# Performance work log

Hardware: AMD Instinct MI355X
Metric: run time of the kernel (lower is better)

## Reference

```python
import jax, jax.numpy as jnp
import numpy as np
import math

ANSWER_LEN = 11; D_MODEL = 6; FFN_DIM = 3; HEAD_DIM = 3; MAX_SEQ_LEN = 34
N_HEADS = 2; POS_DIM = 3; TOK_DIM = 3; VOCAB_SIZE = 14; MAX_DIGITS = 10
EOS_TOKEN = 12; EQUALS_TOKEN = 11; PAD_TOKEN = 13; PLUS_TOKEN = 10
B, T = 65536, 34


def _spiral(i, period):
    return (math.cos(2 * math.pi * i / period), math.sin(2 * math.pi * i / period), i / max(period - 1, 1))


def _build_pos_enc():
    N_POS = 10
    pe = np.zeros((MAX_SEQ_LEN, POS_DIM), dtype=np.float32)
    for i in range(MAX_DIGITS):
        pe[i] = _spiral(i, N_POS)
    for i in range(MAX_DIGITS):
        pe[11 + i] = _spiral(i, N_POS)
    for i in range(min(ANSWER_LEN, N_POS)):
        pe[22 + i] = _spiral(i, N_POS)
    pe[32] = [0.0, 0.0, 1.5]
    pe[10] = [2.0, 0.0, -1.0]
    pe[21] = [0.0, 2.0, -1.0]
    pe[33] = [-2.0, 0.0, -1.0]
    return pe


def _build_tok_emb():
    emb = np.zeros((VOCAB_SIZE, TOK_DIM), dtype=np.float32)
    for d in range(10):
        emb[d] = _spiral(d, 10)
    emb[PLUS_TOKEN] = [2.0, 0.0, -1.0]
    emb[EQUALS_TOKEN] = [0.0, 2.0, -1.0]
    emb[EOS_TOKEN] = [-2.0, 0.0, -1.0]
    emb[PAD_TOKEN] = [0.0, -2.0, -1.0]
    return emb


def setup_inputs() -> dict:
    key = jax.random.key(0)
    ks = jax.random.split(key, 12)
    H = N_HEADS * HEAD_DIM  # 6

    def lin(k, out_d, in_d):
        bound = 1.0 / math.sqrt(in_d)
        return jax.random.uniform(k, (out_d, in_d), jnp.float32, -bound, bound)

    return {
        'idx': jax.random.randint(ks[0], (B, T), 0, VOCAB_SIZE),
        'tok_emb': jnp.asarray(_build_tok_emb()),
        'pos_enc': jnp.asarray(_build_pos_enc()),
        'q_w': lin(ks[1], H, POS_DIM),
        'k_w': lin(ks[2], H, POS_DIM),
        'v_w': lin(ks[3], H, TOK_DIM),
        'out_w': lin(ks[4], D_MODEL, H),
        'ln1_g': jnp.ones((D_MODEL,)), 'ln1_b': jnp.zeros((D_MODEL,)),
        'ln2_g': jnp.ones((D_MODEL,)), 'ln2_b': jnp.zeros((D_MODEL,)),
        'lnf_g': jnp.ones((D_MODEL,)), 'lnf_b': jnp.zeros((D_MODEL,)),
        'ffn_w1': lin(ks[5], FFN_DIM, D_MODEL),
        'ffn_b1': jax.random.uniform(ks[6], (FFN_DIM,), jnp.float32, -1/math.sqrt(D_MODEL), 1/math.sqrt(D_MODEL)),
        'ffn_w2': lin(ks[7], D_MODEL, FFN_DIM),
        'ffn_b2': jax.random.uniform(ks[8], (D_MODEL,), jnp.float32, -1/math.sqrt(FFN_DIM), 1/math.sqrt(FFN_DIM)),
        'head_w': lin(ks[9], TOK_DIM, D_MODEL),
    }


def _ln(x, g, b, eps=1e-5):
    mu = jnp.mean(x, -1, keepdims=True)
    var = jnp.mean((x - mu) ** 2, -1, keepdims=True)
    return (x - mu) * jax.lax.rsqrt(var + eps) * g + b


def reference(idx, tok_emb, pos_enc, q_w, k_w, v_w, out_w,
              ln1_g, ln1_b, ln2_g, ln2_b, lnf_g, lnf_b,
              ffn_w1, ffn_b1, ffn_w2, ffn_b2, head_w):
    b, t = idx.shape
    tok = tok_emb[idx]                              # [B,T,3]
    pos = jnp.broadcast_to(pos_enc[:t][None], (b, t, POS_DIM))
    x = jnp.concatenate([tok, pos], -1)             # [B,T,6]
    h = _ln(x, ln1_g, ln1_b)
    x_tok, x_pos = h[..., :TOK_DIM], h[..., TOK_DIM:]
    q = (x_pos @ q_w.T).reshape(b, t, N_HEADS, HEAD_DIM)
    k = (x_pos @ k_w.T).reshape(b, t, N_HEADS, HEAD_DIM)
    v = (x_tok @ v_w.T).reshape(b, t, N_HEADS, HEAD_DIM)
    attn = jnp.einsum('bqhd,bkhd->bhqk', q, k) / math.sqrt(HEAD_DIM)
    mask = jnp.tril(jnp.ones((t, t), dtype=bool))
    attn = jnp.where(mask[None, None], attn, -jnp.inf)
    attn = jax.nn.softmax(attn, -1)
    out = jnp.einsum('bhqk,bkhd->bqhd', attn, v).reshape(b, t, N_HEADS * HEAD_DIM)
    x = x + out @ out_w.T
    h2 = _ln(x, ln2_g, ln2_b)
    ffn = jax.nn.gelu(h2 @ ffn_w1.T + ffn_b1, approximate=False) @ ffn_w2.T + ffn_b2
    x = x + ffn
    x = _ln(x, lnf_g, lnf_b)
    return (x @ head_w.T) @ tok_emb.T               # [B,T,VOCAB]
```

## Files before the change

kernel.cpp:

```cpp
#include <hip/hip_runtime.h>
#include <math.h>

#define TT  34
#define VV  14
#define BLK 256


__global__ __launch_bounds__(BLK) void addtx_fwd(
    const int*   __restrict__ idx,
    const float* __restrict__ tok_emb,
    const float* __restrict__ pos_enc,
    const float* __restrict__ q_w,
    const float* __restrict__ k_w,
    const float* __restrict__ v_w,
    const float* __restrict__ out_w,
    const float* __restrict__ ln1_g, const float* __restrict__ ln1_b,
    const float* __restrict__ ln2_g, const float* __restrict__ ln2_b,
    const float* __restrict__ lnf_g, const float* __restrict__ lnf_b,
    const float* __restrict__ ffn_w1, const float* __restrict__ ffn_b1,
    const float* __restrict__ ffn_w2, const float* __restrict__ ffn_b2,
    const float* __restrict__ head_w,
    float* __restrict__ out)
{
    __shared__ float4 kvtab[TT * VV * 3];
    __shared__ float  wsm[192];
    __shared__ float  lgs[BLK * VV];

    const int tid = threadIdx.x;
    const int blk = blockIdx.x;

    {
        const int i = tid;
        if (i < 36)       wsm[i] = out_w[i];
        else if (i < 42)  wsm[i] = ln2_g[i - 36];
        else if (i < 48)  wsm[i] = ln2_b[i - 42];
        else if (i < 66)  wsm[i] = ffn_w1[i - 48];
        else if (i < 69)  wsm[i] = ffn_b1[i - 66];
        else if (i < 87)  wsm[i] = ffn_w2[i - 69];
        else if (i < 93)  wsm[i] = ffn_b2[i - 87];
        else if (i < 99)  wsm[i] = lnf_g[i - 93];
        else if (i < 105) wsm[i] = lnf_b[i - 99];
        else if (i < 189) {
            const int j = i - 105, v = j / 6, d = j - v * 6;
            wsm[i] = head_w[0 * 6 + d] * tok_emb[v * 3 + 0]
                   + head_w[1 * 6 + d] * tok_emb[v * 3 + 1]
                   + head_w[2 * 6 + d] * tok_emb[v * 3 + 2];
        }
    }

    const float rs3 = 0.57735026918962576f;
    for (int e = tid; e < TT * VV; e += BLK) {
        const int pos = e / VV, id = e - pos * VV;
        float x[6];
        x[0] = tok_emb[id * 3 + 0]; x[1] = tok_emb[id * 3 + 1]; x[2] = tok_emb[id * 3 + 2];
        x[3] = pos_enc[pos * 3 + 0]; x[4] = pos_enc[pos * 3 + 1]; x[5] = pos_enc[pos * 3 + 2];
        float mu = (x[0] + x[1] + x[2] + x[3] + x[4] + x[5]) * (1.0f / 6.0f);
        float var = 0.0f;
        #pragma unroll
        for (int d = 0; d < 6; ++d) { float dd = x[d] - mu; var += dd * dd; }
        const float rstd = rsqrtf(var * (1.0f / 6.0f) + 1e-5f);
        float h[6];
        #pragma unroll
        for (int d = 0; d < 6; ++d) h[d] = (x[d] - mu) * rstd * ln1_g[d] + ln1_b[d];
        float kk[6], vvv[6];
        #pragma unroll
        for (int r = 0; r < 6; ++r) {
            kk[r]  = (h[3] * k_w[r * 3 + 0] + h[4] * k_w[r * 3 + 1] + h[5] * k_w[r * 3 + 2]) * rs3;
            vvv[r] =  h[0] * v_w[r * 3 + 0] + h[1] * v_w[r * 3 + 1] + h[2] * v_w[r * 3 + 2];
        }
        kvtab[e * 3 + 0] = make_float4(kk[0], kk[1], kk[2], kk[3]);
        kvtab[e * 3 + 1] = make_float4(kk[4], kk[5], vvv[0], vvv[1]);
        kvtab[e * 3 + 2] = make_float4(vvv[2], vvv[3], vvv[4], vvv[5]);
    }
    __syncthreads();

    const int srank = (tid + ((blk & 3) << 6)) & (BLK - 1);
    const int r0 = (blk * BLK) % TT;
    int rem = srank, dsel = 0, ksel = 0, found = 0;
    #pragma unroll 1
    for (int tau = 0; tau < TT; ++tau) {
        int dlt = tau - r0; if (dlt < 0) dlt += TT;
        const int c = (dlt < (BLK % TT)) ? (BLK / TT + 1) : (BLK / TT);
        if (!found) {
            if (rem < c) { dsel = dlt; ksel = rem; found = 1; }
            else rem -= c;
        }
    }
    const int il   = dsel + ksel * TT;
    const int flat = blk * BLK + il;
    const int b    = flat / TT;
    const int t    = flat - b * TT;
    const int* __restrict__ row = idx + b * TT;

    float x[6];
    {
        const int mid = row[t];
        x[0] = tok_emb[mid * 3 + 0]; x[1] = tok_emb[mid * 3 + 1]; x[2] = tok_emb[mid * 3 + 2];
        x[3] = pos_enc[t * 3 + 0];   x[4] = pos_enc[t * 3 + 1];   x[5] = pos_enc[t * 3 + 2];
    }
    float q[6];
    {
        float mu = (x[0] + x[1] + x[2] + x[3] + x[4] + x[5]) * (1.0f / 6.0f);
        float var = 0.0f;
        #pragma unroll
        for (int d = 0; d < 6; ++d) { float dd = x[d] - mu; var += dd * dd; }
        const float rstd = rsqrtf(var * (1.0f / 6.0f) + 1e-5f);
        float h[6];
        #pragma unroll
        for (int d = 0; d < 6; ++d) h[d] = (x[d] - mu) * rstd * ln1_g[d] + ln1_b[d];
        #pragma unroll
        for (int r = 0; r < 6; ++r)
            q[r] = h[3] * q_w[r * 3 + 0] + h[4] * q_w[r * 3 + 1] + h[5] * q_w[r * 3 + 2];
    }

    float l0 = 0.f, l1 = 0.f;
    float a0 = 0.f, a1 = 0.f, a2 = 0.f, a3 = 0.f, a4 = 0.f, a5 = 0.f;
    int ebase = 0;
    for (int s = 0; s <= t; ++s) {
        const int ids = row[s];
        const float4* e4 = &kvtab[(ebase + ids) * 3];
        const float4 ka = e4[0];
        const float4 kb = e4[1];
        const float4 vb = e4[2];
        const float sc0 = q[0] * ka.x + q[1] * ka.y + q[2] * ka.z;
        const float sc1 = q[3] * ka.w + q[4] * kb.x + q[5] * kb.y;
        const float p0 = __expf(sc0);
        const float p1 = __expf(sc1);
        l0 += p0; l1 += p1;
        a0 += p0 * kb.z; a1 += p0 * kb.w; a2 += p0 * vb.x;
        a3 += p1 * vb.y; a4 += p1 * vb.z; a5 += p1 * vb.w;
        ebase += VV;
    }
    const float i0 = 1.0f / l0, i1 = 1.0f / l1;
    const float o6[6] = { a0 * i0, a1 * i0, a2 * i0, a3 * i1, a4 * i1, a5 * i1 };

    #pragma unroll
    for (int d = 0; d < 6; ++d) {
        float s = x[d];
        #pragma unroll
        for (int j = 0; j < 6; ++j) s += o6[j] * wsm[d * 6 + j];
        x[d] = s;
    }

    {
        float mu = (x[0] + x[1] + x[2] + x[3] + x[4] + x[5]) * (1.0f / 6.0f);
        float var = 0.0f;
        #pragma unroll
        for (int d = 0; d < 6; ++d) { float dd = x[d] - mu; var += dd * dd; }
        const float rstd = rsqrtf(var * (1.0f / 6.0f) + 1e-5f);
        float h2[6];
        #pragma unroll
        for (int d = 0; d < 6; ++d) h2[d] = (x[d] - mu) * rstd * wsm[36 + d] + wsm[42 + d];
        float g3[3];
        #pragma unroll
        for (int i = 0; i < 3; ++i) {
            float f = wsm[66 + i];
            #pragma unroll
            for (int d = 0; d < 6; ++d) f += h2[d] * wsm[48 + i * 6 + d];
            g3[i] = 0.5f * f * (1.0f + erff(f * 0.70710678118654752f));
        }
        #pragma unroll
        for (int d = 0; d < 6; ++d) {
            float s = x[d] + wsm[87 + d];
            #pragma unroll
            for (int i = 0; i < 3; ++i) s += g3[i] * wsm[69 + d * 3 + i];
            x[d] = s;
        }
    }

    {
        float mu = (x[0] + x[1] + x[2] + x[3] + x[4] + x[5]) * (1.0f / 6.0f);
        float var = 0.0f;
        #pragma unroll
        for (int d = 0; d < 6; ++d) { float dd = x[d] - mu; var += dd * dd; }
        const float rstd = rsqrtf(var * (1.0f / 6.0f) + 1e-5f);
        float xf[6];
        #pragma unroll
        for (int d = 0; d < 6; ++d) xf[d] = (x[d] - mu) * rstd * wsm[93 + d] + wsm[99 + d];
        #pragma unroll
        for (int v = 0; v < VV; ++v) {
            float s = 0.0f;
            #pragma unroll
            for (int d = 0; d < 6; ++d) s += xf[d] * wsm[105 + v * 6 + d];
            lgs[il * VV + v] = s;
        }
    }
    __syncthreads();

    float* __restrict__ ob = out + (size_t)blk * (BLK * VV);
    #pragma unroll
    for (int j = 0; j < VV; ++j)
        ob[j * BLK + tid] = lgs[j * BLK + tid];
}

extern "C" void kernel_launch(void* const* d_in, const int* in_sizes, int n_in,
                              void* d_out, int out_size, void* d_ws, size_t ws_size,
                              hipStream_t stream) {
    const int*   idx     = (const int*)  d_in[0];
    const float* tok_emb = (const float*)d_in[1];
    const float* pos_enc = (const float*)d_in[2];
    const float* q_w     = (const float*)d_in[3];
    const float* k_w     = (const float*)d_in[4];
    const float* v_w     = (const float*)d_in[5];
    const float* out_w   = (const float*)d_in[6];
    const float* ln1_g   = (const float*)d_in[7];
    const float* ln1_b   = (const float*)d_in[8];
    const float* ln2_g   = (const float*)d_in[9];
    const float* ln2_b   = (const float*)d_in[10];
    const float* lnf_g   = (const float*)d_in[11];
    const float* lnf_b   = (const float*)d_in[12];
    const float* ffn_w1  = (const float*)d_in[13];
    const float* ffn_b1  = (const float*)d_in[14];
    const float* ffn_w2  = (const float*)d_in[15];
    const float* ffn_b2  = (const float*)d_in[16];
    const float* head_w  = (const float*)d_in[17];
    float* out = (float*)d_out;

    const int n = in_sizes[0];
    const int blocks = n / BLK;
    addtx_fwd<<<blocks, BLK, 0, stream>>>(idx, tok_emb, pos_enc, q_w, k_w, v_w, out_w,
                                          ln1_g, ln1_b, ln2_g, ln2_b, lnf_g, lnf_b,
                                          ffn_w1, ffn_b1, ffn_w2, ffn_b2, head_w, out);
}
```

Before: 256.7 us.

## Remap work so each lane owns a sequence and processes several query positions

Each block now handles 64 sequences. Each wave covers a slice of 4 (or 6) query positions, and each lane owns one sequence, so K/V table lookups in the causal attention loop are shared across several queries held in registers. Token indices are staged in padded shared memory, embeddings and ln1/q weights are cached in shared memory, and exp is replaced with exp2 using pre-scaled queries. Logits are written straight to global memory with float4 stores instead of being staged in shared memory. The cost is higher register pressure, imbalance between waves (the last wave does more work), and per-lane strided global stores that may coalesce poorly.

```diff
diff --git a/kernel.cpp b/kernel.cpp
--- a/kernel.cpp
+++ b/kernel.cpp
@@ -1,19 +1,145 @@
 #include <hip/hip_runtime.h>
 #include <math.h>
 
-#define TT  34
-#define VV  14
-#define BLK 256
-
-
-__global__ __launch_bounds__(BLK) void addtx_fwd(
+#define TT   34
+#define VV   14
+#define NROW 64
+#define BLK  512
+
+
+__device__ __forceinline__ void epi_t(int t, int id, const float* a,
+                                      const float* wsm, const float* stab,
+                                      float* lg) {
+    const float i0 = 1.0f / a[0], i1 = 1.0f / a[1];
+    const float o6[6] = { a[2]*i0, a[3]*i0, a[4]*i0, a[5]*i1, a[6]*i1, a[7]*i1 };
+    float x[6];
+    x[0] = stab[id*3+0]; x[1] = stab[id*3+1]; x[2] = stab[id*3+2];
+    x[3] = stab[42+t*3+0]; x[4] = stab[42+t*3+1]; x[5] = stab[42+t*3+2];
+    #pragma unroll
+    for (int d = 0; d < 6; ++d) {
+        float s = x[d];
+        #pragma unroll
+        for (int j = 0; j < 6; ++j) s += o6[j] * wsm[d*6+j];
+        x[d] = s;
+    }
+    {
+        float mu = (x[0]+x[1]+x[2]+x[3]+x[4]+x[5]) * (1.0f/6.0f);
+        float var = 0.f;
+        #pragma unroll
+        for (int d = 0; d < 6; ++d) { float dd = x[d]-mu; var += dd*dd; }
+        const float rstd = rsqrtf(var*(1.0f/6.0f) + 1e-5f);
+        float h2[6];
+        #pragma unroll
+        for (int d = 0; d < 6; ++d) h2[d] = (x[d]-mu)*rstd*wsm[36+d] + wsm[42+d];
+        float g3[3];
+        #pragma unroll
+        for (int i = 0; i < 3; ++i) {
+            float f = wsm[66+i];
+            #pragma unroll
+            for (int d = 0; d < 6; ++d) f += h2[d]*wsm[48+i*6+d];
+            g3[i] = 0.5f * f * (1.0f + erff(f*0.70710678118654752f));
+        }
+        #pragma unroll
+        for (int d = 0; d < 6; ++d) {
+            float s = x[d] + wsm[87+d];
+            #pragma unroll
+            for (int i = 0; i < 3; ++i) s += g3[i]*wsm[69+d*3+i];
+            x[d] = s;
+        }
+    }
+    {
+        float mu = (x[0]+x[1]+x[2]+x[3]+x[4]+x[5]) * (1.0f/6.0f);
+        float var = 0.f;
+        #pragma unroll
+        for (int d = 0; d < 6; ++d) { float dd = x[d]-mu; var += dd*dd; }
+        const float rstd = rsqrtf(var*(1.0f/6.0f) + 1e-5f);
+        float xf[6];
+        #pragma unroll
+        for (int d = 0; d < 6; ++d) xf[d] = (x[d]-mu)*rstd*wsm[93+d] + wsm[99+d];
+        #pragma unroll
+        for (int v = 0; v < VV; ++v) {
+            float s = 0.f;
+            #pragma unroll
+            for (int d = 0; d < 6; ++d) s += xf[d]*wsm[105+v*6+d];
+            lg[v] = s;
+        }
+    }
+}
+
+#define ATT_BODY(J) do { \
+    float sc0 = q[J][0]*ka.x + q[J][1]*ka.y + q[J][2]*ka.z; \
+    float sc1 = q[J][3]*ka.w + q[J][4]*kb.x + q[J][5]*kb.y; \
+    float p0 = exp2f(sc0); \
+    float p1 = exp2f(sc1); \
+    acc[J][0] += p0;       acc[J][1] += p1; \
+    acc[J][2] += p0*kb.z;  acc[J][3] += p0*kb.w;  acc[J][4] += p0*vb.x; \
+    acc[J][5] += p1*vb.y;  acc[J][6] += p1*vb.z;  acc[J][7] += p1*vb.w; \
+} while (0)
+
+template<int G>
+__device__ __forceinline__ void slot_run(int t0, const int* __restrict__ lrow,
+                                         const float4* __restrict__ kvt,
+                                         const float* __restrict__ wsm,
+                                         const float* __restrict__ stab,
+                                         float* __restrict__ outp) {
+    const float qs = 1.4426950408889634f;
+    float q[G][6];
+    float acc[G][8];
+    #pragma unroll
+    for (int j = 0; j < G; ++j) {
+        const int t = t0 + j;
+        const int id = lrow[t];
+        const float x0 = stab[id*3+0], x1 = stab[id*3+1], x2 = stab[id*3+2];
+        const float x3 = stab[42+t*3+0], x4 = stab[42+t*3+1], x5 = stab[42+t*3+2];
+        const float mu = (x0+x1+x2+x3+x4+x5) * (1.0f/6.0f);
+        const float d0=x0-mu,d1=x1-mu,d2=x2-mu,d3=x3-mu,d4=x4-mu,d5=x5-mu;
+        const float var = d0*d0+d1*d1+d2*d2+d3*d3+d4*d4+d5*d5;
+        const float rstd = rsqrtf(var*(1.0f/6.0f) + 1e-5f);
+        const float h3 = d3*rstd*stab[147] + stab[153];
+        const float h4 = d4*rstd*stab[148] + stab[154];
+        const float h5 = d5*rstd*stab[149] + stab[155];
+        #pragma unroll
+        for (int r = 0; r < 6; ++r)
+            q[j][r] = (h3*stab[156+r*3] + h4*stab[156+r*3+1] + h5*stab[156+r*3+2]) * qs;
+        #pragma unroll
+        for (int k = 0; k < 8; ++k) acc[j][k] = 0.f;
+    }
+    for (int s = 0; s <= t0; ++s) {
+        const int ids = lrow[s];
+        const float4* e4 = &kvt[(s*VV + ids)*3];
+        const float4 ka = e4[0], kb = e4[1], vb = e4[2];
+        #pragma unroll
+        for (int j = 0; j < G; ++j) ATT_BODY(j);
+    }
+    #pragma unroll
+    for (int u = 1; u < G; ++u) {
+        const int s = t0 + u;
+        const int ids = lrow[s];
+        const float4* e4 = &kvt[(s*VV + ids)*3];
+        const float4 ka = e4[0], kb = e4[1], vb = e4[2];
+        #pragma unroll
+        for (int j = u; j < G; ++j) ATT_BODY(j);
+    }
+    #pragma unroll
+    for (int p = 0; p < G/2; ++p) {
+        alignas(16) float lg[28];
+        #pragma unroll
+        for (int h = 0; h < 2; ++h) {
+            const int j = 2*p + h, t = t0 + j;
+            epi_t(t, lrow[t], acc[j], wsm, stab, &lg[14*h]);
+        }
+        float4* d4 = (float4*)(outp + (t0 + 2*p)*VV);
+        const float4* s4 = (const float4*)lg;
+        #pragma unroll
+        for (int w = 0; w < 7; ++w) d4[w] = s4[w];
+    }
+}
+
+__global__ __launch_bounds__(BLK, 4) void addtx_fwd(
     const int*   __restrict__ idx,
-    const float* __restrict__ tok_emb,
-    const float* __restrict__ pos_enc,
-    const float* __restrict__ q_w,
-    const float* __restrict__ k_w,
-    const float* __restrict__ v_w,
-    const float* __restrict__ out_w,
+    const float* __restrict__ tok_emb, const float* __restrict__ pos_enc,
+    const float* __restrict__ q_w, const float* __restrict__ k_w,
+    const float* __restrict__ v_w, const float* __restrict__ out_w,
     const float* __restrict__ ln1_g, const float* __restrict__ ln1_b,
     const float* __restrict__ ln2_g, const float* __restrict__ ln2_b,
     const float* __restrict__ lnf_g, const float* __restrict__ lnf_b,
@@ -22,175 +148,83 @@
     const float* __restrict__ head_w,
     float* __restrict__ out)
 {
-    __shared__ float4 kvtab[TT * VV * 3];
+    __shared__ float4 kvtab[TT*VV*3];
     __shared__ float  wsm[192];
-    __shared__ float  lgs[BLK * VV];
+    __shared__ float  stab[176];
+    __shared__ int    lidx[NROW*35];
 
     const int tid = threadIdx.x;
     const int blk = blockIdx.x;
 
-    {
+    if (tid < 189) {
         const int i = tid;
-        if (i < 36)       wsm[i] = out_w[i];
-        else if (i < 42)  wsm[i] = ln2_g[i - 36];
-        else if (i < 48)  wsm[i] = ln2_b[i - 42];
-        else if (i < 66)  wsm[i] = ffn_w1[i - 48];
-        else if (i < 69)  wsm[i] = ffn_b1[i - 66];
-        else if (i < 87)  wsm[i] = ffn_w2[i - 69];
-        else if (i < 93)  wsm[i] = ffn_b2[i - 87];
-        else if (i < 99)  wsm[i] = lnf_g[i - 93];
-        else if (i < 105) wsm[i] = lnf_b[i - 99];
-        else if (i < 189) {
-            const int j = i - 105, v = j / 6, d = j - v * 6;
-            wsm[i] = head_w[0 * 6 + d] * tok_emb[v * 3 + 0]
-                   + head_w[1 * 6 + d] * tok_emb[v * 3 + 1]
-                   + head_w[2 * 6 + d] * tok_emb[v * 3 + 2];
-        }
-    }
-
-    const float rs3 = 0.57735026918962576f;
-    for (int e = tid; e < TT * VV; e += BLK) {
-        const int pos = e / VV, id = e - pos * VV;
+        float w;
+        if (i < 36)       w = out_w[i];
+        else if (i < 42)  w = ln2_g[i-36];
+        else if (i < 48)  w = ln2_b[i-42];
+        else if (i < 66)  w = ffn_w1[i-48];
+        else if (i < 69)  w = ffn_b1[i-66];
+        else if (i < 87)  w = ffn_w2[i-69];
+        else if (i < 93)  w = ffn_b2[i-87];
+        else if (i < 99)  w = lnf_g[i-93];
+        else if (i < 105) w = lnf_b[i-99];
+        else {
+            const int j = i-105, v = j/6, d = j-v*6;
+            w = head_w[0*6+d]*tok_emb[v*3+0] + head_w[1*6+d]*tok_emb[v*3+1]
+              + head_w[2*6+d]*tok_emb[v*3+2];
+        }
+        wsm[i] = w;
+    } else if (tid < 192 + 174 && tid >= 192) {
+        const int i = tid - 192;
+        float w;
+        if (i < 42)        w = tok_emb[i];
+        else if (i < 144)  w = pos_enc[i-42];
+        else if (i < 150)  w = ln1_g[i-144];
+        else if (i < 156)  w = ln1_b[i-150];
+        else               w = q_w[i-156];
+        stab[i] = w;
+    }
+
+    if (tid < TT*VV) {
+        const int e = tid;
+        const int pos = e / VV, id = e - pos*VV;
+        const float rs3 = 0.57735026918962576f;
         float x[6];
-        x[0] = tok_emb[id * 3 + 0]; x[1] = tok_emb[id * 3 + 1]; x[2] = tok_emb[id * 3 + 2];
-        x[3] = pos_enc[pos * 3 + 0]; x[4] = pos_enc[pos * 3 + 1]; x[5] = pos_enc[pos * 3 + 2];
-        float mu = (x[0] + x[1] + x[2] + x[3] + x[4] + x[5]) * (1.0f / 6.0f);
-        float var = 0.0f;
-        #pragma unroll
-        for (int d = 0; d < 6; ++d) { float dd = x[d] - mu; var += dd * dd; }
-        const float rstd = rsqrtf(var * (1.0f / 6.0f) + 1e-5f);
+        x[0]=tok_emb[id*3+0]; x[1]=tok_emb[id*3+1]; x[2]=tok_emb[id*3+2];
+        x[3]=pos_enc[pos*3+0]; x[4]=pos_enc[pos*3+1]; x[5]=pos_enc[pos*3+2];
+        float mu = (x[0]+x[1]+x[2]+x[3]+x[4]+x[5]) * (1.0f/6.0f);
+        float var = 0.f;
+        #pragma unroll
+        for (int d = 0; d < 6; ++d) { float dd = x[d]-mu; var += dd*dd; }
+        const float rstd = rsqrtf(var*(1.0f/6.0f) + 1e-5f);
         float h[6];
         #pragma unroll
-        for (int d = 0; d < 6; ++d) h[d] = (x[d] - mu) * rstd * ln1_g[d] + ln1_b[d];
-        float kk[6], vvv[6];
+        for (int d = 0; d < 6; ++d) h[d] = (x[d]-mu)*rstd*ln1_g[d] + ln1_b[d];
+        float kk[6], vv[6];
         #pragma unroll
         for (int r = 0; r < 6; ++r) {
-            kk[r]  = (h[3] * k_w[r * 3 + 0] + h[4] * k_w[r * 3 + 1] + h[5] * k_w[r * 3 + 2]) * rs3;
-            vvv[r] =  h[0] * v_w[r * 3 + 0] + h[1] * v_w[r * 3 + 1] + h[2] * v_w[r * 3 + 2];
-        }
-        kvtab[e * 3 + 0] = make_float4(kk[0], kk[1], kk[2], kk[3]);
-        kvtab[e * 3 + 1] = make_float4(kk[4], kk[5], vvv[0], vvv[1]);
-        kvtab[e * 3 + 2] = make_float4(vvv[2], vvv[3], vvv[4], vvv[5]);
+            kk[r] = (h[3]*k_w[r*3+0] + h[4]*k_w[r*3+1] + h[5]*k_w[r*3+2]) * rs3;
+            vv[r] =  h[0]*v_w[r*3+0] + h[1]*v_w[r*3+1] + h[2]*v_w[r*3+2];
+        }
+        kvtab[e*3+0] = make_float4(kk[0],kk[1],kk[2],kk[3]);
+        kvtab[e*3+1] = make_float4(kk[4],kk[5],vv[0],vv[1]);
+        kvtab[e*3+2] = make_float4(vv[2],vv[3],vv[4],vv[5]);
+    }
+
+    for (int j = tid; j < NROW*TT; j += BLK) {
+        const int r = j / TT, c = j - r*TT;
+        lidx[r*35 + c] = idx[(size_t)blk * (NROW*TT) + j];
     }
     __syncthreads();
 
-    const int srank = (tid + ((blk & 3) << 6)) & (BLK - 1);
-    const int r0 = (blk * BLK) % TT;
-    int rem = srank, dsel = 0, ksel = 0, found = 0;
-    #pragma unroll 1
-    for (int tau = 0; tau < TT; ++tau) {
-        int dlt = tau - r0; if (dlt < 0) dlt += TT;
-        const int c = (dlt < (BLK % TT)) ? (BLK / TT + 1) : (BLK / TT);
-        if (!found) {
-            if (rem < c) { dsel = dlt; ksel = rem; found = 1; }
-            else rem -= c;
-        }
-    }
-    const int il   = dsel + ksel * TT;
-    const int flat = blk * BLK + il;
-    const int b    = flat / TT;
-    const int t    = flat - b * TT;
-    const int* __restrict__ row = idx + b * TT;
-
-    float x[6];
-    {
-        const int mid = row[t];
-        x[0] = tok_emb[mid * 3 + 0]; x[1] = tok_emb[mid * 3 + 1]; x[2] = tok_emb[mid * 3 + 2];
-        x[3] = pos_enc[t * 3 + 0];   x[4] = pos_enc[t * 3 + 1];   x[5] = pos_enc[t * 3 + 2];
-    }
-    float q[6];
-    {
-        float mu = (x[0] + x[1] + x[2] + x[3] + x[4] + x[5]) * (1.0f / 6.0f);
-        float var = 0.0f;
-        #pragma unroll
-        for (int d = 0; d < 6; ++d) { float dd = x[d] - mu; var += dd * dd; }
-        const float rstd = rsqrtf(var * (1.0f / 6.0f) + 1e-5f);
-        float h[6];
-        #pragma unroll
-        for (int d = 0; d < 6; ++d) h[d] = (x[d] - mu) * rstd * ln1_g[d] + ln1_b[d];
-        #pragma unroll
-        for (int r = 0; r < 6; ++r)
-            q[r] = h[3] * q_w[r * 3 + 0] + h[4] * q_w[r * 3 + 1] + h[5] * q_w[r * 3 + 2];
-    }
-
-    float l0 = 0.f, l1 = 0.f;
-    float a0 = 0.f, a1 = 0.f, a2 = 0.f, a3 = 0.f, a4 = 0.f, a5 = 0.f;
-    int ebase = 0;
-    for (int s = 0; s <= t; ++s) {
-        const int ids = row[s];
-        const float4* e4 = &kvtab[(ebase + ids) * 3];
-        const float4 ka = e4[0];
-        const float4 kb = e4[1];
-        const float4 vb = e4[2];
-        const float sc0 = q[0] * ka.x + q[1] * ka.y + q[2] * ka.z;
-        const float sc1 = q[3] * ka.w + q[4] * kb.x + q[5] * kb.y;
-        const float p0 = __expf(sc0);
-        const float p1 = __expf(sc1);
-        l0 += p0; l1 += p1;
-        a0 += p0 * kb.z; a1 += p0 * kb.w; a2 += p0 * vb.x;
-        a3 += p1 * vb.y; a4 += p1 * vb.z; a5 += p1 * vb.w;
-        ebase += VV;
-    }
-    const float i0 = 1.0f / l0, i1 = 1.0f / l1;
-    const float o6[6] = { a0 * i0, a1 * i0, a2 * i0, a3 * i1, a4 * i1, a5 * i1 };
-
-    #pragma unroll
-    for (int d = 0; d < 6; ++d) {
-        float s = x[d];
-        #pragma unroll
-        for (int j = 0; j < 6; ++j) s += o6[j] * wsm[d * 6 + j];
-        x[d] = s;
-    }
-
-    {
-        float mu = (x[0] + x[1] + x[2] + x[3] + x[4] + x[5]) * (1.0f / 6.0f);
-        float var = 0.0f;
-        #pragma unroll
-        for (int d = 0; d < 6; ++d) { float dd = x[d] - mu; var += dd * dd; }
-        const float rstd = rsqrtf(var * (1.0f / 6.0f) + 1e-5f);
-        float h2[6];
-        #pragma unroll
-        for (int d = 0; d < 6; ++d) h2[d] = (x[d] - mu) * rstd * wsm[36 + d] + wsm[42 + d];
-        float g3[3];
-        #pragma unroll
-        for (int i = 0; i < 3; ++i) {
-            float f = wsm[66 + i];
-            #pragma unroll
-            for (int d = 0; d < 6; ++d) f += h2[d] * wsm[48 + i * 6 + d];
-            g3[i] = 0.5f * f * (1.0f + erff(f * 0.70710678118654752f));
-        }
-        #pragma unroll
-        for (int d = 0; d < 6; ++d) {
-            float s = x[d] + wsm[87 + d];
-            #pragma unroll
-            for (int i = 0; i < 3; ++i) s += g3[i] * wsm[69 + d * 3 + i];
-            x[d] = s;
-        }
-    }
-
-    {
-        float mu = (x[0] + x[1] + x[2] + x[3] + x[4] + x[5]) * (1.0f / 6.0f);
-        float var = 0.0f;
-        #pragma unroll
-        for (int d = 0; d < 6; ++d) { float dd = x[d] - mu; var += dd * dd; }
-        const float rstd = rsqrtf(var * (1.0f / 6.0f) + 1e-5f);
-        float xf[6];
-        #pragma unroll
-        for (int d = 0; d < 6; ++d) xf[d] = (x[d] - mu) * rstd * wsm[93 + d] + wsm[99 + d];
-        #pragma unroll
-        for (int v = 0; v < VV; ++v) {
-            float s = 0.0f;
-            #pragma unroll
-            for (int d = 0; d < 6; ++d) s += xf[d] * wsm[105 + v * 6 + d];
-            lgs[il * VV + v] = s;
-        }
-    }
-    __syncthreads();
-
-    float* __restrict__ ob = out + (size_t)blk * (BLK * VV);
-    #pragma unroll
-    for (int j = 0; j < VV; ++j)
-        ob[j * BLK + tid] = lgs[j * BLK + tid];
+    const int wv = tid >> 6, lane = tid & 63;
+    const int t0 = wv * 4;
+    const int b  = blk * NROW + lane;
+    const int* lrow = &lidx[lane*35];
+    float* outp = out + (size_t)b * (TT*VV);
+
+    if (wv < 7) slot_run<4>(t0, lrow, kvtab, wsm, stab, outp);
+    else        slot_run<6>(t0, lrow, kvtab, wsm, stab, outp);
 }
 
 extern "C" void kernel_launch(void* const* d_in, const int* in_sizes, int n_in,
@@ -216,8 +250,8 @@
     const float* head_w  = (const float*)d_in[17];
     float* out = (float*)d_out;
 
-    const int n = in_sizes[0];
-    const int blocks = n / BLK;
+    const int rows   = in_sizes[0] / TT;
+    const int blocks = rows / NROW;
     addtx_fwd<<<blocks, BLK, 0, stream>>>(idx, tok_emb, pos_enc, q_w, k_w, v_w, out_w,
                                           ln1_g, ln1_b, ln2_g, ln2_b, lnf_g, lnf_b,
                                           ffn_w1, ffn_b1, ffn_w2, ffn_b2, head_w, out);
```

New measurement: 745.9 us. 191% more time.
